# Kernel tuning notes

Hardware: AMD Instinct MI355X
Metric: run time of the kernel (lower is better)

The kernel has to match this reference:

```python
import jax, jax.numpy as jnp
import numpy as np

D_FEAT = 6
HID = 256
T = 60
B_DAYS = 4
STOCKS = 512
TRAIN_DAYS = 240
K_DAY = 10
N_NEIGHBOR = 10
SLOPE = 0.01  # nn.LeakyReLU default


def setup_inputs() -> dict:
    key = jax.random.key(0)
    ks = jax.random.split(key, 32)
    g = lambda i, shape, s=0.05: (jax.random.normal(ks[i], shape, dtype=jnp.float32) * s)
    inp = jax.random.normal(ks[0], (B_DAYS, STOCKS, D_FEAT * T), dtype=jnp.float32)
    train_hidden = jax.random.normal(ks[1], (TRAIN_DAYS, STOCKS, HID), dtype=jnp.float32)
    train_hidden_day = jax.random.normal(ks[2], (TRAIN_DAYS, HID), dtype=jnp.float32)
    return {
        "inp": inp,
        "train_hidden": train_hidden,
        "train_hidden_day": train_hidden_day,
        # GRU layer 0 (input D_FEAT) and layer 1 (input HID); gates [r,z,n] stacked -> 3*HID
        "W_ih0": g(3, (3 * HID, D_FEAT)), "W_hh0": g(4, (3 * HID, HID)),
        "b_ih0": g(5, (3 * HID,)), "b_hh0": g(6, (3 * HID,)),
        "W_ih1": g(7, (3 * HID, HID)), "W_hh1": g(8, (3 * HID, HID)),
        "b_ih1": g(9, (3 * HID,)), "b_hh1": g(10, (3 * HID,)),
        # lins MLP 256->512->512->256
        "lin0_W": g(11, (512, HID)), "lin0_b": g(12, (512,)),
        "lin1_W": g(13, (512, 512)), "lin1_b": g(14, (512,)),
        "lin2_W": g(15, (HID, 512)), "lin2_b": g(16, (HID,)),
        # projections (no bias) and output head
        "proj1_W": g(17, (HID, HID)), "proj2_W": g(18, (HID, HID)),
        "fc_W": g(19, (1, 2 * HID)), "fc_b": g(20, (1,)),
    }


def _leaky(x):
    return jnp.where(x >= 0, x, SLOPE * x)


def _gru_layer(x, W_ih, W_hh, b_ih, b_hh):
    # x: [N, T, in] -> [N, T, HID]
    xW = jnp.einsum('nti,gi->ntg', x, W_ih) + b_ih  # precompute input gates
    def step(h, xw):
        gh = h @ W_hh.T + b_hh
        xr, xz, xn = jnp.split(xw, 3, axis=-1)
        hr, hz, hn = jnp.split(gh, 3, axis=-1)
        r = jax.nn.sigmoid(xr + hr)
        z = jax.nn.sigmoid(xz + hz)
        n = jnp.tanh(xn + r * hn)
        h = (1.0 - z) * n + z * h
        return h, h
    h0 = jnp.zeros((x.shape[0], W_hh.shape[1]), x.dtype)
    _, hs = jax.lax.scan(step, h0, jnp.swapaxes(xW, 0, 1))
    return jnp.swapaxes(hs, 0, 1)


def _cos_sim(x, y):
    xy = x @ y.T
    xn = jnp.sqrt(jnp.sum(x * x, axis=1))[:, None]
    yn = jnp.sqrt(jnp.sum(y * y, axis=1))[:, None]
    cs = xy / (xn @ yn.T)
    return jnp.where(jnp.isnan(cs), 0.0, cs)


def reference(inp, train_hidden, train_hidden_day,
              W_ih0, W_hh0, b_ih0, b_hh0, W_ih1, W_hh1, b_ih1, b_hh1,
              lin0_W, lin0_b, lin1_W, lin1_b, lin2_W, lin2_b,
              proj1_W, proj2_W, fc_W, fc_b):
    B, S = inp.shape[0], inp.shape[1]
    x = inp.reshape(B * S, D_FEAT, -1).transpose(0, 2, 1)  # [N, T, d_feat]
    h = _gru_layer(x, W_ih0, W_hh0, b_ih0, b_hh0)
    h = _gru_layer(h, W_ih1, W_hh1, b_ih1, b_hh1)
    out = h[:, -1, :]                                      # [N, HID]
    mb = _leaky(out @ lin0_W.T + lin0_b)
    mb = _leaky(mb @ lin1_W.T + lin1_b)
    mb = _leaky(mb @ lin2_W.T + lin2_b)                    # mini_batch_out [N, HID]
    mb_day = jnp.mean(mb.reshape(B, S, -1), axis=1)        # [B, HID]
    day_sim = _cos_sim(mb_day, train_hidden_day)           # [B, TRAIN_DAYS]
    _, day_idx = jax.lax.top_k(day_sim, K_DAY)             # [B, K_DAY]
    sample = train_hidden[day_idx].reshape(-1, train_hidden.shape[-1])  # [B*K_DAY*S, HID]
    q = mb @ proj1_W.T
    kh = sample @ proj2_W.T
    cs = _cos_sim(q, kh)                                   # [N, B*K_DAY*S]
    vals, idx = jax.lax.top_k(cs, N_NEIGHBOR)              # per-row top-k (distinct cols)
    # sparse mask (ones/n_neighbor) * cos_sim, then sparse @ kh == weighted gather-sum
    agg = jnp.einsum('nk,nkh->nh', vals / N_NEIGHBOR, kh[idx])
    cat = jnp.concatenate([mb, agg], axis=1)               # [N, 2*HID]
    y = (cat @ fc_W.T + fc_b).squeeze(-1)
    return y.reshape(B, -1)
```

## Files before the change

### kernel.cpp

```cpp
#include <hip/hip_runtime.h>
#include <cmath>
#include <cstdint>

#define D_FEAT 6
#define T_SEQ  60
#define HID    256
#define G3     768
#define NROW   2048
#define NSAMP  20480

__device__ __forceinline__ float sigmoidf_(float x) { return 1.0f / (1.0f + expf(-x)); }

struct PrepArgs {
  const float* src[9];
  float* dst[9];
  int N[9], K[9], ro[9];
};

__global__ void prep_weights(PrepArgs a) {
  int seg = blockIdx.y;
  const float* S = a.src[seg];
  float* D = a.dst[seg];
  int N = a.N[seg], K = a.K[seg], ro = a.ro[seg];
  int total = N * K;
  for (int i = blockIdx.x * blockDim.x + threadIdx.x; i < total; i += gridDim.x * blockDim.x) {
    int n = i / K, k = i - n * K;
    D[(size_t)(k + ro) * N + n] = S[i];
  }
}

__device__ __forceinline__ void kloop256(const float* __restrict__ A,
                                         const float* __restrict__ B,
                                         float (&acc)[3][8])
{
  float4 Aa[4][2];
  float  Bb[2][12];
#pragma unroll
  for (int c = 0; c < 4; ++c) {
    Aa[c][0] = *(const float4*)(A + c * 8);
    Aa[c][1] = *(const float4*)(A + c * 8 + 4);
  }
#pragma unroll
  for (int c = 0; c < 4; ++c)
#pragma unroll
    for (int u = 0; u < 3; ++u)
      Bb[0][c * 3 + u] = B[(size_t)c * G3 + u * 256];

  for (int kb = 0; kb < 256; kb += 8) {
    {
      const float* p = B + (size_t)(kb + 4) * G3;
#pragma unroll
      for (int c = 0; c < 4; ++c)
#pragma unroll
        for (int u = 0; u < 3; ++u)
          Bb[1][c * 3 + u] = p[(size_t)c * G3 + u * 256];
    }
#pragma unroll
    for (int c = 0; c < 4; ++c) {
      float4 alo = Aa[c][0], ahi = Aa[c][1];
      int kn = kb + 4 + c;
      Aa[c][0] = *(const float4*)(A + kn * 8);
      Aa[c][1] = *(const float4*)(A + kn * 8 + 4);
#pragma unroll
      for (int u = 0; u < 3; ++u) {
        float b = Bb[0][c * 3 + u];
        acc[u][0] += alo.x * b; acc[u][1] += alo.y * b;
        acc[u][2] += alo.z * b; acc[u][3] += alo.w * b;
        acc[u][4] += ahi.x * b; acc[u][5] += ahi.y * b;
        acc[u][6] += ahi.z * b; acc[u][7] += ahi.w * b;
      }
    }
    {
      int kw = (kb + 8) & 255;
      const float* p = B + (size_t)kw * G3;
#pragma unroll
      for (int c = 0; c < 4; ++c)
#pragma unroll
        for (int u = 0; u < 3; ++u)
          Bb[0][c * 3 + u] = p[(size_t)c * G3 + u * 256];
    }
#pragma unroll
    for (int c = 0; c < 4; ++c) {
      float4 alo = Aa[c][0], ahi = Aa[c][1];
      int kn = (kb + 8 + c) & 255;
      Aa[c][0] = *(const float4*)(A + kn * 8);
      Aa[c][1] = *(const float4*)(A + kn * 8 + 4);
#pragma unroll
      for (int u = 0; u < 3; ++u) {
        float b = Bb[1][c * 3 + u];
        acc[u][0] += alo.x * b; acc[u][1] += alo.y * b;
        acc[u][2] += alo.z * b; acc[u][3] += alo.w * b;
        acc[u][4] += ahi.x * b; acc[u][5] += ahi.y * b;
        acc[u][6] += ahi.z * b; acc[u][7] += ahi.w * b;
      }
    }
  }
}

__global__ __launch_bounds__(256, 1)
void gru_fused(const float* __restrict__ inp, const float* __restrict__ WThh0,
               const float* __restrict__ WTcat, const float* __restrict__ WTih0,
               const float* __restrict__ bih0, const float* __restrict__ bhh0,
               const float* __restrict__ bih1, const float* __restrict__ bhh1,
               float* __restrict__ hrow)
{
  __shared__ float h0A[2048], h0B[2048];
  __shared__ float h1A[2048], h1B[2048];
  __shared__ float xls[2880];

  const int tid = threadIdx.x;
  const int m0 = blockIdx.x * 8;

  for (int c = tid; c < 2880; c += 256) {
    int row = c / 360, it = c - row * 360;
    xls[it * 8 + row] = inp[(size_t)(m0 + row) * 360 + it];
  }
  for (int c = tid; c < 2048; c += 256) { h0A[c] = 0.f; h1A[c] = 0.f; }

  float h0c[8], h1c[8];
#pragma unroll
  for (int r = 0; r < 8; ++r) { h0c[r] = 0.f; h1c[r] = 0.f; }

  float b_ih0[3], b_hh0[3], b_ih1[3], b_hh1[3];
#pragma unroll
  for (int u = 0; u < 3; ++u) {
    int o = u * 256 + tid;
    b_ih0[u] = bih0[o]; b_hh0[u] = bhh0[o];
    b_ih1[u] = bih1[o]; b_hh1[u] = bhh1[o];
  }
  __syncthreads();

  const float* Bhh0 = WThh0 + tid;
  const float* Bc0  = WTcat + tid;
  const float* Bc1  = WTcat + (size_t)256 * G3 + tid;

  for (int t = 0; t < T_SEQ; ++t) {
    const float* h0cur = (t & 1) ? h0B : h0A;
    float*       h0nxt = (t & 1) ? h0A : h0B;
    const float* h1cur = (t & 1) ? h1B : h1A;
    float*       h1nxt = (t & 1) ? h1A : h1B;

    float xw[3][8];
#pragma unroll
    for (int u = 0; u < 3; ++u)
#pragma unroll
      for (int r = 0; r < 8; ++r) xw[u][r] = b_ih0[u];
#pragma unroll
    for (int i = 0; i < 6; ++i) {
      float4 xlo = *(const float4*)&xls[(i * 60 + t) * 8];
      float4 xhi = *(const float4*)&xls[(i * 60 + t) * 8 + 4];
#pragma unroll
      for (int u = 0; u < 3; ++u) {
        float b = WTih0[i * G3 + u * 256 + tid];
        xw[u][0] += xlo.x * b; xw[u][1] += xlo.y * b;
        xw[u][2] += xlo.z * b; xw[u][3] += xlo.w * b;
        xw[u][4] += xhi.x * b; xw[u][5] += xhi.y * b;
        xw[u][6] += xhi.z * b; xw[u][7] += xhi.w * b;
      }
    }
    float gh[3][8];
#pragma unroll
    for (int u = 0; u < 3; ++u)
#pragma unroll
      for (int r = 0; r < 8; ++r) gh[u][r] = 0.f;
    kloop256(h0cur, Bhh0, gh);

    {
      float hn[8];
#pragma unroll
      for (int r = 0; r < 8; ++r) {
        float rr = sigmoidf_(xw[0][r] + (gh[0][r] + b_hh0[0]));
        float zz = sigmoidf_(xw[1][r] + (gh[1][r] + b_hh0[1]));
        float nn = tanhf(xw[2][r] + rr * (gh[2][r] + b_hh0[2]));
        h0c[r] = (1.f - zz) * nn + zz * h0c[r];
        hn[r] = h0c[r];
      }
      *(float4*)&h0nxt[tid * 8]     = *(float4*)&hn[0];
      *(float4*)&h0nxt[tid * 8 + 4] = *(float4*)&hn[4];
    }
    __syncthreads();

    float acc[3][8];
#pragma unroll
    for (int u = 0; u < 3; ++u)
#pragma unroll
      for (int r = 0; r < 8; ++r) acc[u][r] = 0.f;
    kloop256(h0nxt, Bc0, acc);
    float xn8[8];
#pragma unroll
    for (int r = 0; r < 8; ++r) { xn8[r] = acc[2][r]; acc[2][r] = 0.f; }
    kloop256(h1cur, Bc1, acc);

    {
      float hn[8];
#pragma unroll
      for (int r = 0; r < 8; ++r) {
        float rr = sigmoidf_((acc[0][r] + b_ih1[0]) + b_hh1[0]);
        float zz = sigmoidf_((acc[1][r] + b_ih1[1]) + b_hh1[1]);
        float nn = tanhf((xn8[r] + b_ih1[2]) + rr * (acc[2][r] + b_hh1[2]));
        h1c[r] = (1.f - zz) * nn + zz * h1c[r];
        hn[r] = h1c[r];
      }
      *(float4*)&h1nxt[tid * 8]     = *(float4*)&hn[0];
      *(float4*)&h1nxt[tid * 8 + 4] = *(float4*)&hn[4];
    }
    __syncthreads();
  }

#pragma unroll
  for (int r = 0; r < 8; ++r)
    hrow[(size_t)(m0 + r) * 256 + tid] = h1c[r];
}

__global__ __launch_bounds__(256, 2)
void gemm_act(const float* __restrict__ A, const int* __restrict__ rowsrc,
              const float* __restrict__ WT, const float* __restrict__ bias,
              float* __restrict__ C, int M, int N, int K, int act)
{
  __shared__ float4 As4[128 * 32];
  const int tx = threadIdx.x, ty = threadIdx.y;
  const int tid = ty * 32 + tx;
  const int n0 = blockIdx.x * 32, m0 = blockIdx.y * 32;
  const int K4 = K >> 2;

  for (int c = tid; c < K4 * 32; c += 256) {
    int k4 = c % K4, m = c / K4;
    int row = m0 + m;
    if (rowsrc) row = rowsrc[row];
    As4[k4 * 32 + m] = *(const float4*)(A + (size_t)row * K + k4 * 4);
  }
  __syncthreads();

  float acc[4] = {0,0,0,0};
  const int n = n0 + tx;
  const float* pb = WT + n;

  float bc[4], bn_[4];
#pragma unroll
  for (int kk = 0; kk < 4; ++kk) bc[kk] = pb[(size_t)kk * N];
  for (int k4 = 0; k4 < K4; ++k4) {
    int nk4 = (k4 + 1 < K4) ? (k4 + 1) : 0;
    const float* pn = pb + (size_t)nk4 * 4 * N;
#pragma unroll
    for (int kk = 0; kk < 4; ++kk) bn_[kk] = pn[(size_t)kk * N];
    float4 a0 = As4[k4 * 32 + ty * 4 + 0];
    float4 a1 = As4[k4 * 32 + ty * 4 + 1];
    float4 a2 = As4[k4 * 32 + ty * 4 + 2];
    float4 a3 = As4[k4 * 32 + ty * 4 + 3];
#pragma unroll
    for (int kk = 0; kk < 4; ++kk) {
      float b = bc[kk];
      acc[0] += ((const float*)&a0)[kk] * b;
      acc[1] += ((const float*)&a1)[kk] * b;
      acc[2] += ((const float*)&a2)[kk] * b;
      acc[3] += ((const float*)&a3)[kk] * b;
    }
#pragma unroll
    for (int q = 0; q < 4; ++q) bc[q] = bn_[q];
  }
  float bb = bias ? bias[n] : 0.f;
#pragma unroll
  for (int r = 0; r < 4; ++r) {
    float v = acc[r] + bb;
    if (act) v = (v >= 0.f) ? v : 0.01f * v;
    C[(size_t)(m0 + ty * 4 + r) * N + n] = v;
  }
}

__global__ void mbday_part(const float* __restrict__ mbf, float* __restrict__ part) {
  int d = blockIdx.x, sl = blockIdx.y, c = threadIdx.x;
  float s = 0.f;
  int base = d * 512 + sl * 64;
  for (int st = 0; st < 64; ++st) s += mbf[(size_t)(base + st) * 256 + c];
  part[(size_t)(d * 8 + sl) * 256 + c] = s;
}

__global__ void mbday_fin(const float* __restrict__ part, float* __restrict__ mbday) {
  int d = blockIdx.x, c = threadIdx.x;
  float s = 0.f;
#pragma unroll
  for (int p = 0; p < 8; ++p) s += part[(size_t)(d * 8 + p) * 256 + c];
  mbday[d * 256 + c] = s * (1.0f / 512.0f);
}

__global__ void daytopk_kernel(const float* __restrict__ mbday, const float* __restrict__ thd,
                               int* __restrict__ dayidx) {
  __shared__ float mbs[256];
  __shared__ float sim[256];
  __shared__ float red[256];
  __shared__ int   redi[256];
  const int d = blockIdx.x, t = threadIdx.x;
  mbs[t] = mbday[d * 256 + t];
  __syncthreads();
  red[t] = mbs[t] * mbs[t];
  __syncthreads();
  for (int o = 128; o; o >>= 1) { if (t < o) red[t] += red[t + o]; __syncthreads(); }
  float xn = sqrtf(red[0]);
  float v = -INFINITY;
  if (t < 240) {
    float dot = 0.f, yn2 = 0.f;
    for (int k = 0; k < 256; ++k) {
      float y = thd[t * 256 + k];
      dot += mbs[k] * y;
      yn2 += y * y;
    }
    float den = xn * sqrtf(yn2);
    v = (den > 0.f) ? dot / den : 0.f;
  }
  sim[t] = v;
  __syncthreads();
  for (int it = 0; it < 10; ++it) {
    red[t] = sim[t]; redi[t] = t;
    __syncthreads();
    for (int o = 128; o; o >>= 1) {
      if (t < o) {
        if (red[t + o] > red[t] || (red[t + o] == red[t] && redi[t + o] < redi[t])) {
          red[t] = red[t + o]; redi[t] = redi[t + o];
        }
      }
      __syncthreads();
    }
    if (t == 0) { int bi = redi[0]; dayidx[d * 10 + it] = bi; sim[bi] = -INFINITY; }
    __syncthreads();
  }
}

__global__ void rowsrc_kernel(const int* __restrict__ dayidx, int* __restrict__ rowsrc) {
  int r = blockIdx.x * 256 + threadIdx.x;
  if (r < NSAMP) rowsrc[r] = dayidx[r >> 9] * 512 + (r & 511);
}

__global__ void rownorm_kernel(const float* __restrict__ X, float* __restrict__ out, int rows) {
  int w = threadIdx.x >> 6;
  int lane = threadIdx.x & 63;
  int row = blockIdx.x * 4 + w;
  if (row >= rows) return;
  float4 x = *(const float4*)(X + (size_t)row * 256 + lane * 4);
  float s = x.x * x.x + x.y * x.y + x.z * x.z + x.w * x.w;
#pragma unroll
  for (int o = 32; o; o >>= 1) s += __shfl_down(s, o, 64);
  if (lane == 0) out[row] = sqrtf(s);
}

__global__ void qnorm_kernel(float* __restrict__ q, const float* __restrict__ qn) {
  int i = blockIdx.x * 256 + threadIdx.x;
  int row = i >> 8;
  float n = qn[row];
  q[i] = (n > 0.f) ? q[i] / n : 0.f;
}

__global__ void khT_kernel(const float* __restrict__ kh, const float* __restrict__ khn,
                           float* __restrict__ khT) {
  __shared__ float tile[32][33];
  int jb = blockIdx.x * 32;
  int kb = blockIdx.y * 32;
  int tx = threadIdx.x & 31, tyy = threadIdx.x >> 5;
  for (int rr = tyy; rr < 32; rr += 8) {
    float n = khn[jb + rr];
    float v = kh[(size_t)(jb + rr) * 256 + kb + tx];
    tile[rr][tx] = (n > 0.f) ? v / n : 0.f;
  }
  __syncthreads();
  for (int rr = tyy; rr < 32; rr += 8) {
    khT[(size_t)(kb + rr) * NSAMP + jb + tx] = tile[tx][rr];
  }
}

__global__ __launch_bounds__(256, 4)
void csmax_kernel(const float* __restrict__ qh, const float* __restrict__ khT,
                  float* __restrict__ topvp, int* __restrict__ topip)
{
  __shared__ float4 qs[256][2];
  __shared__ float csch[8 * 512];
  const int tid = threadIdx.x;
  const int split = blockIdx.x & 7;
  const int m0 = (blockIdx.x >> 3) * 8;
  {
    int k = tid;
    float4 v0, v1;
    v0.x = qh[(size_t)(m0 + 0) * 256 + k]; v0.y = qh[(size_t)(m0 + 1) * 256 + k];
    v0.z = qh[(size_t)(m0 + 2) * 256 + k]; v0.w = qh[(size_t)(m0 + 3) * 256 + k];
    v1.x = qh[(size_t)(m0 + 4) * 256 + k]; v1.y = qh[(size_t)(m0 + 5) * 256 + k];
    v1.z = qh[(size_t)(m0 + 6) * 256 + k]; v1.w = qh[(size_t)(m0 + 7) * 256 + k];
    qs[k][0] = v0; qs[k][1] = v1;
  }
  __syncthreads();
  const int lane = tid & 63;
  const int wv = tid >> 6;

  float tv0[10], tv1[10];
  int   tj0[10], tj1[10];
  int   tn0 = 0, tn1 = 0;
  float tmv0 = -INFINITY, tmv1 = -INFINITY;
  int   tmi0 = 0, tmi1 = 0;

  auto process_row = [&](int r, float (&tv)[10], int (&tj)[10], int& tn,
                         float& tmv, int& tmi, int jb) {
    float4 c0 = *(const float4*)&csch[r * 512 + lane * 8];
    float4 c1 = *(const float4*)&csch[r * 512 + lane * 8 + 4];
    float cv[8] = {c0.x, c0.y, c0.z, c0.w, c1.x, c1.y, c1.z, c1.w};
    const int cj0 = jb + lane * 8;
    while (true) {
      float bv = -INFINITY; int bj = 0x7fffffff;
#pragma unroll
      for (int u = 0; u < 8; ++u) {
        if (cv[u] > bv) { bv = cv[u]; bj = cj0 + u; }
      }
#pragma unroll
      for (int o = 32; o; o >>= 1) {
        float ov = __shfl_down(bv, o, 64);
        int   oj = __shfl_down(bj, o, 64);
        if (ov > bv || (ov == bv && oj < bj)) { bv = ov; bj = oj; }
      }
      bv = __shfl(bv, 0, 64); bj = __shfl(bj, 0, 64);
      bool take;
      if (tn < 10) take = true;
      else take = (bv > tmv) || (bv == tmv && bj < tmi);
      if (!take) break;
      if (tn < 10) {
#pragma unroll
        for (int s = 0; s < 10; ++s) if (s == tn) { tv[s] = bv; tj[s] = bj; }
        tn++;
        if (tn == 10) {
          float mv = tv[0]; int mi = tj[0];
#pragma unroll
          for (int s = 1; s < 10; ++s) {
            bool w = (tv[s] < mv) || (tv[s] == mv && tj[s] > mi);
            if (w) { mv = tv[s]; mi = tj[s]; }
          }
          tmv = mv; tmi = mi;
        }
      } else {
        int ms = 0; float mv = tv[0]; int mi = tj[0];
#pragma unroll
        for (int s = 1; s < 10; ++s) {
          bool w = (tv[s] < mv) || (tv[s] == mv && tj[s] > mi);
          if (w) { ms = s; mv = tv[s]; mi = tj[s]; }
        }
#pragma unroll
        for (int s = 0; s < 10; ++s) if (s == ms) { tv[s] = bv; tj[s] = bj; }
        mv = tv[0]; mi = tj[0];
#pragma unroll
        for (int s = 1; s < 10; ++s) {
          bool w = (tv[s] < mv) || (tv[s] == mv && tj[s] > mi);
          if (w) { mv = tv[s]; mi = tj[s]; }
        }
        tmv = mv; tmi = mi;
      }
#pragma unroll
      for (int u = 0; u < 8; ++u) if (cj0 + u == bj) cv[u] = -INFINITY;
    }
  };

  for (int ci = 0; ci < 5; ++ci) {
    const int ch = split * 5 + ci;
    const int jb = ch * 512;
    float acc[8][2];
#pragma unroll
    for (int r = 0; r < 8; ++r) { acc[r][0] = 0.f; acc[r][1] = 0.f; }
    const float* kp = khT + jb + tid;

    float b0c[4], b1c[4], b0n[4], b1n[4];
#pragma unroll
    for (int kk = 0; kk < 4; ++kk) {
      b0c[kk] = kp[(size_t)kk * NSAMP];
      b1c[kk] = kp[(size_t)kk * NSAMP + 256];
    }
    for (int k4 = 0; k4 < 64; ++k4) {
      int nk4 = (k4 + 1) & 63;
      const float* pn = kp + (size_t)nk4 * 4 * NSAMP;
#pragma unroll
      for (int kk = 0; kk < 4; ++kk) {
        b0n[kk] = pn[(size_t)kk * NSAMP];
        b1n[kk] = pn[(size_t)kk * NSAMP + 256];
      }
#pragma unroll
      for (int kk = 0; kk < 4; ++kk) {
        float4 qa = qs[k4 * 4 + kk][0];
        float4 qb = qs[k4 * 4 + kk][1];
        float b0 = b0c[kk], b1 = b1c[kk];
        acc[0][0] += qa.x * b0; acc[1][0] += qa.y * b0; acc[2][0] += qa.z * b0; acc[3][0] += qa.w * b0;
        acc[4][0] += qb.x * b0; acc[5][0] += qb.y * b0; acc[6][0] += qb.z * b0; acc[7][0] += qb.w * b0;
        acc[0][1] += qa.x * b1; acc[1][1] += qa.y * b1; acc[2][1] += qa.z * b1; acc[3][1] += qa.w * b1;
        acc[4][1] += qb.x * b1; acc[5][1] += qb.y * b1; acc[6][1] += qb.z * b1; acc[7][1] += qb.w * b1;
      }
#pragma unroll
      for (int q = 0; q < 4; ++q) { b0c[q] = b0n[q]; b1c[q] = b1n[q]; }
    }
    __syncthreads();
#pragma unroll
    for (int r = 0; r < 8; ++r) {
      csch[r * 512 + tid] = acc[r][0];
      csch[r * 512 + 256 + tid] = acc[r][1];
    }
    __syncthreads();
    process_row(wv,     tv0, tj0, tn0, tmv0, tmi0, jb);
    process_row(wv + 4, tv1, tj1, tn1, tmv1, tmi1, jb);
  }
  __syncthreads();

  if (lane == 0) {
    int row0 = m0 + wv;
#pragma unroll
    for (int s = 0; s < 10; ++s) {
      topvp[(size_t)row0 * 80 + split * 10 + s] = tv0[s];
      topip[(size_t)row0 * 80 + split * 10 + s] = tj0[s];
    }
    int row1 = m0 + wv + 4;
#pragma unroll
    for (int s = 0; s < 10; ++s) {
      topvp[(size_t)row1 * 80 + split * 10 + s] = tv1[s];
      topip[(size_t)row1 * 80 + split * 10 + s] = tj1[s];
    }
  }
}

__global__ void merge_topk(const float* __restrict__ topvp, const int* __restrict__ topip,
                           float* __restrict__ topv, int* __restrict__ topi)
{
  const int wv = threadIdx.x >> 6;
  const int lane = threadIdx.x & 63;
  const int row = blockIdx.x * 4 + wv;
  float v0 = topvp[(size_t)row * 80 + lane];
  int   i0 = topip[(size_t)row * 80 + lane];
  float v1 = (lane < 16) ? topvp[(size_t)row * 80 + 64 + lane] : -INFINITY;
  int   i1 = (lane < 16) ? topip[(size_t)row * 80 + 64 + lane] : 0x7fffffff;
  for (int s = 0; s < 10; ++s) {
    float bv = v0; int bj = i0;
    if (v1 > bv || (v1 == bv && i1 < bj)) { bv = v1; bj = i1; }
#pragma unroll
    for (int o = 1; o < 64; o <<= 1) {
      float ov = __shfl_xor(bv, o, 64);
      int   oj = __shfl_xor(bj, o, 64);
      if (ov > bv || (ov == bv && oj < bj)) { bv = ov; bj = oj; }
    }
    if (lane == 0) { topv[row * 10 + s] = bv; topi[row * 10 + s] = bj; }
    if (i0 == bj) { v0 = -INFINITY; i0 = 0x7fffffff; }
    if (i1 == bj) { v1 = -INFINITY; i1 = 0x7fffffff; }
  }
}

__global__ void final_kernel(const float* __restrict__ mb, const float* __restrict__ kh,
                             const float* __restrict__ topv, const int* __restrict__ topi,
                             const float* __restrict__ fcW, const float* __restrict__ fcb,
                             float* __restrict__ y)
{
  __shared__ float red[256];
  int n = blockIdx.x, c = threadIdx.x;
  float agg = 0.f;
#pragma unroll
  for (int k = 0; k < 10; ++k) {
    float w = topv[n * 10 + k] / 10.0f;
    int idx = topi[n * 10 + k];
    agg += w * kh[(size_t)idx * 256 + c];
  }
  float val = fcW[c] * mb[(size_t)n * 256 + c] + fcW[256 + c] * agg;
  red[c] = val;
  __syncthreads();
  for (int o = 128; o; o >>= 1) { if (c < o) red[c] += red[c + o]; __syncthreads(); }
  if (c == 0) y[n] = red[0] + fcb[0];
}

extern "C" void kernel_launch(void* const* d_in, const int* in_sizes, int n_in,
                              void* d_out, int out_size, void* d_ws, size_t ws_size,
                              hipStream_t stream)
{
  const float* inp    = (const float*)d_in[0];
  const float* trainh = (const float*)d_in[1];
  const float* thd    = (const float*)d_in[2];
  const float* Wih0   = (const float*)d_in[3];
  const float* Whh0   = (const float*)d_in[4];
  const float* bih0   = (const float*)d_in[5];
  const float* bhh0   = (const float*)d_in[6];
  const float* Wih1   = (const float*)d_in[7];
  const float* Whh1   = (const float*)d_in[8];
  const float* bih1   = (const float*)d_in[9];
  const float* bhh1   = (const float*)d_in[10];
  const float* lin0W  = (const float*)d_in[11];
  const float* lin0b  = (const float*)d_in[12];
  const float* lin1W  = (const float*)d_in[13];
  const float* lin1b  = (const float*)d_in[14];
  const float* lin2W  = (const float*)d_in[15];
  const float* lin2b  = (const float*)d_in[16];
  const float* p1W    = (const float*)d_in[17];
  const float* p2W    = (const float*)d_in[18];
  const float* fcW    = (const float*)d_in[19];
  const float* fcb    = (const float*)d_in[20];

  float* ws = (float*)d_ws;
  float* WT_hh0 = ws + 0;
  float* WTcat  = ws + 196608;
  float* WT_l0  = ws + 589824;
  float* WT_l1  = ws + 720896;
  float* WT_l2  = ws + 983040;
  float* WT_p1  = ws + 1114112;
  float* WT_p2  = ws + 1179648;
  float* hrow   = ws + 1245184;
  float* mb1    = ws + 3342336;
  float* mb2    = ws + 4390912;
  float* mbf    = ws + 5439488;
  float* mbday  = ws + 5963776;
  float* qbuf   = ws + 5964800;
  float* kh     = ws + 6489088;
  float* khT    = ws + 11731968;
  float* khn    = ws + 16974848;
  float* qn     = ws + 16995328;
  float* topv   = ws + 16997376;
  int*   dayidx = (int*)(ws + 17017856);
  int*   rowsrc = (int*)(ws + 17017920);
  int*   topi   = (int*)(ws + 17038400);
  float* topvp  = mb1;
  int*   topip  = (int*)(mb1 + 163840);
  float* WT_ih0 = mb2;
  float* mbpart = mb2;

  PrepArgs pa;
  pa.src[0] = Whh0;  pa.dst[0] = WT_hh0; pa.N[0] = 768; pa.K[0] = 256; pa.ro[0] = 0;
  pa.src[1] = Wih1;  pa.dst[1] = WTcat;  pa.N[1] = 768; pa.K[1] = 256; pa.ro[1] = 0;
  pa.src[2] = Whh1;  pa.dst[2] = WTcat;  pa.N[2] = 768; pa.K[2] = 256; pa.ro[2] = 256;
  pa.src[3] = lin0W; pa.dst[3] = WT_l0;  pa.N[3] = 512; pa.K[3] = 256; pa.ro[3] = 0;
  pa.src[4] = lin1W; pa.dst[4] = WT_l1;  pa.N[4] = 512; pa.K[4] = 512; pa.ro[4] = 0;
  pa.src[5] = lin2W; pa.dst[5] = WT_l2;  pa.N[5] = 256; pa.K[5] = 512; pa.ro[5] = 0;
  pa.src[6] = p1W;   pa.dst[6] = WT_p1;  pa.N[6] = 256; pa.K[6] = 256; pa.ro[6] = 0;
  pa.src[7] = p2W;   pa.dst[7] = WT_p2;  pa.N[7] = 256; pa.K[7] = 256; pa.ro[7] = 0;
  pa.src[8] = Wih0;  pa.dst[8] = WT_ih0; pa.N[8] = 768; pa.K[8] = 6;   pa.ro[8] = 0;
  prep_weights<<<dim3(64, 9), dim3(256), 0, stream>>>(pa);

  gru_fused<<<256, 256, 0, stream>>>(inp, WT_hh0, WTcat, WT_ih0, bih0, bhh0, bih1, bhh1, hrow);

  gemm_act<<<dim3(16, 64), dim3(32, 8), 0, stream>>>(hrow, nullptr, WT_l0, lin0b, mb1, 2048, 512, 256, 1);
  gemm_act<<<dim3(16, 64), dim3(32, 8), 0, stream>>>(mb1, nullptr, WT_l1, lin1b, mb2, 2048, 512, 512, 1);
  gemm_act<<<dim3(8, 64),  dim3(32, 8), 0, stream>>>(mb2, nullptr, WT_l2, lin2b, mbf, 2048, 256, 512, 1);

  mbday_part<<<dim3(4, 8), 256, 0, stream>>>(mbf, mbpart);
  mbday_fin<<<4, 256, 0, stream>>>(mbpart, mbday);
  daytopk_kernel<<<4, 256, 0, stream>>>(mbday, thd, dayidx);
  rowsrc_kernel<<<80, 256, 0, stream>>>(dayidx, rowsrc);

  gemm_act<<<dim3(8, 640), dim3(32, 8), 0, stream>>>(trainh, rowsrc, WT_p2, nullptr, kh, 20480, 256, 256, 0);
  gemm_act<<<dim3(8, 64),  dim3(32, 8), 0, stream>>>(mbf, nullptr, WT_p1, nullptr, qbuf, 2048, 256, 256, 0);

  rownorm_kernel<<<5120, 256, 0, stream>>>(kh, khn, 20480);
  rownorm_kernel<<<512, 256, 0, stream>>>(qbuf, qn, 2048);
  qnorm_kernel<<<2048, 256, 0, stream>>>(qbuf, qn);
  khT_kernel<<<dim3(640, 8), 256, 0, stream>>>(kh, khn, khT);

  csmax_kernel<<<2048, 256, 0, stream>>>(qbuf, khT, topvp, topip);
  merge_topk<<<512, 256, 0, stream>>>(topvp, topip, topv, topi);
  final_kernel<<<2048, 256, 0, stream>>>(mbf, kh, topv, topi, fcW, fcb, (float*)d_out);

  (void)in_sizes; (void)n_in; (void)out_size; (void)ws_size;
}
```

Before: 3.799 ms.

## Split GRU recurrent K-reduction across two thread halves with shared-memory exchange

The fused GRU kernel now launches 512 threads per block. Each half computes a 128-wide slice of the hidden-dimension reduction, and the partial sums are combined through a padded shared-memory exchange buffer. This doubles the wavefronts per CU so the latency-bound recurrent matvec gets more parallelism. In exchange it adds two extra block-wide barriers per timestep and leaves the upper half idle during the gate nonlinearities.

```diff
diff --git a/kernel.cpp b/kernel.cpp
--- a/kernel.cpp
+++ b/kernel.cpp
@@ -29,7 +29,7 @@
   }
 }
 
-__device__ __forceinline__ void kloop256(const float* __restrict__ A,
+__device__ __forceinline__ void kloop128(const float* __restrict__ A,
                                          const float* __restrict__ B,
                                          float (&acc)[3][8])
 {
@@ -46,7 +46,7 @@
     for (int u = 0; u < 3; ++u)
       Bb[0][c * 3 + u] = B[(size_t)c * G3 + u * 256];
 
-  for (int kb = 0; kb < 256; kb += 8) {
+  for (int kb = 0; kb < 128; kb += 8) {
     {
       const float* p = B + (size_t)(kb + 4) * G3;
 #pragma unroll
@@ -71,7 +71,7 @@
       }
     }
     {
-      int kw = (kb + 8) & 255;
+      int kw = (kb + 8) & 127;
       const float* p = B + (size_t)kw * G3;
 #pragma unroll
       for (int c = 0; c < 4; ++c)
@@ -82,7 +82,7 @@
 #pragma unroll
     for (int c = 0; c < 4; ++c) {
       float4 alo = Aa[c][0], ahi = Aa[c][1];
-      int kn = (kb + 8 + c) & 255;
+      int kn = (kb + 8 + c) & 127;
       Aa[c][0] = *(const float4*)(A + kn * 8);
       Aa[c][1] = *(const float4*)(A + kn * 8 + 4);
 #pragma unroll
@@ -97,7 +97,7 @@
   }
 }
 
-__global__ __launch_bounds__(256, 1)
+__global__ __launch_bounds__(512, 1)
 void gru_fused(const float* __restrict__ inp, const float* __restrict__ WThh0,
                const float* __restrict__ WTcat, const float* __restrict__ WTih0,
                const float* __restrict__ bih0, const float* __restrict__ bhh0,
@@ -107,15 +107,18 @@
   __shared__ float h0A[2048], h0B[2048];
   __shared__ float h1A[2048], h1B[2048];
   __shared__ float xls[2880];
+  __shared__ float exch[256 * 33];
 
   const int tid = threadIdx.x;
+  const int col = tid & 255;
+  const int half = tid >> 8;
   const int m0 = blockIdx.x * 8;
 
-  for (int c = tid; c < 2880; c += 256) {
+  for (int c = tid; c < 2880; c += 512) {
     int row = c / 360, it = c - row * 360;
     xls[it * 8 + row] = inp[(size_t)(m0 + row) * 360 + it];
   }
-  for (int c = tid; c < 2048; c += 256) { h0A[c] = 0.f; h1A[c] = 0.f; }
+  for (int c = tid; c < 2048; c += 512) { h0A[c] = 0.f; h1A[c] = 0.f; }
 
   float h0c[8], h1c[8];
 #pragma unroll
@@ -124,15 +127,17 @@
   float b_ih0[3], b_hh0[3], b_ih1[3], b_hh1[3];
 #pragma unroll
   for (int u = 0; u < 3; ++u) {
-    int o = u * 256 + tid;
+    int o = u * 256 + col;
     b_ih0[u] = bih0[o]; b_hh0[u] = bhh0[o];
     b_ih1[u] = bih1[o]; b_hh1[u] = bhh1[o];
   }
   __syncthreads();
 
-  const float* Bhh0 = WThh0 + tid;
-  const float* Bc0  = WTcat + tid;
-  const float* Bc1  = WTcat + (size_t)256 * G3 + tid;
+  const int aoff = half * 1024;
+  const float* Bhh0 = WThh0 + (size_t)(half * 128) * G3 + col;
+  const float* Bc0  = WTcat + (size_t)(half * 128) * G3 + col;
+  const float* Bc1  = WTcat + (size_t)(256 + half * 128) * G3 + col;
+  float* exc = exch + col * 33;
 
   for (int t = 0; t < T_SEQ; ++t) {
     const float* h0cur = (t & 1) ? h0B : h0A;
@@ -140,43 +145,55 @@
     const float* h1cur = (t & 1) ? h1B : h1A;
     float*       h1nxt = (t & 1) ? h1A : h1B;
 
+    float gh[3][8];
+#pragma unroll
+    for (int u = 0; u < 3; ++u)
+#pragma unroll
+      for (int r = 0; r < 8; ++r) gh[u][r] = 0.f;
+    kloop128(h0cur + aoff, Bhh0, gh);
+
     float xw[3][8];
-#pragma unroll
-    for (int u = 0; u < 3; ++u)
-#pragma unroll
-      for (int r = 0; r < 8; ++r) xw[u][r] = b_ih0[u];
-#pragma unroll
-    for (int i = 0; i < 6; ++i) {
-      float4 xlo = *(const float4*)&xls[(i * 60 + t) * 8];
-      float4 xhi = *(const float4*)&xls[(i * 60 + t) * 8 + 4];
-#pragma unroll
-      for (int u = 0; u < 3; ++u) {
-        float b = WTih0[i * G3 + u * 256 + tid];
-        xw[u][0] += xlo.x * b; xw[u][1] += xlo.y * b;
-        xw[u][2] += xlo.z * b; xw[u][3] += xlo.w * b;
-        xw[u][4] += xhi.x * b; xw[u][5] += xhi.y * b;
-        xw[u][6] += xhi.z * b; xw[u][7] += xhi.w * b;
-      }
-    }
-    float gh[3][8];
-#pragma unroll
-    for (int u = 0; u < 3; ++u)
-#pragma unroll
-      for (int r = 0; r < 8; ++r) gh[u][r] = 0.f;
-    kloop256(h0cur, Bhh0, gh);
-
-    {
+    if (half == 0) {
+#pragma unroll
+      for (int u = 0; u < 3; ++u)
+#pragma unroll
+        for (int r = 0; r < 8; ++r) xw[u][r] = b_ih0[u];
+#pragma unroll
+      for (int i = 0; i < 6; ++i) {
+        float4 xlo = *(const float4*)&xls[(i * 60 + t) * 8];
+        float4 xhi = *(const float4*)&xls[(i * 60 + t) * 8 + 4];
+#pragma unroll
+        for (int u = 0; u < 3; ++u) {
+          float b = WTih0[i * G3 + u * 256 + col];
+          xw[u][0] += xlo.x * b; xw[u][1] += xlo.y * b;
+          xw[u][2] += xlo.z * b; xw[u][3] += xlo.w * b;
+          xw[u][4] += xhi.x * b; xw[u][5] += xhi.y * b;
+          xw[u][6] += xhi.z * b; xw[u][7] += xhi.w * b;
+        }
+      }
+    } else {
+#pragma unroll
+      for (int u = 0; u < 3; ++u)
+#pragma unroll
+        for (int r = 0; r < 8; ++r) exc[u * 8 + r] = gh[u][r];
+    }
+    __syncthreads();
+
+    if (half == 0) {
       float hn[8];
 #pragma unroll
       for (int r = 0; r < 8; ++r) {
-        float rr = sigmoidf_(xw[0][r] + (gh[0][r] + b_hh0[0]));
-        float zz = sigmoidf_(xw[1][r] + (gh[1][r] + b_hh0[1]));
-        float nn = tanhf(xw[2][r] + rr * (gh[2][r] + b_hh0[2]));
+        float g0 = gh[0][r] + exc[r];
+        float g1 = gh[1][r] + exc[8 + r];
+        float g2 = gh[2][r] + exc[16 + r];
+        float rr = sigmoidf_(xw[0][r] + (g0 + b_hh0[0]));
+        float zz = sigmoidf_(xw[1][r] + (g1 + b_hh0[1]));
+        float nn = tanhf(xw[2][r] + rr * (g2 + b_hh0[2]));
         h0c[r] = (1.f - zz) * nn + zz * h0c[r];
         hn[r] = h0c[r];
       }
-      *(float4*)&h0nxt[tid * 8]     = *(float4*)&hn[0];
-      *(float4*)&h0nxt[tid * 8 + 4] = *(float4*)&hn[4];
+      *(float4*)&h0nxt[col * 8]     = *(float4*)&hn[0];
+      *(float4*)&h0nxt[col * 8 + 4] = *(float4*)&hn[4];
     }
     __syncthreads();
 
@@ -185,31 +202,48 @@
     for (int u = 0; u < 3; ++u)
 #pragma unroll
       for (int r = 0; r < 8; ++r) acc[u][r] = 0.f;
-    kloop256(h0nxt, Bc0, acc);
+    kloop128(h0nxt + aoff, Bc0, acc);
     float xn8[8];
 #pragma unroll
     for (int r = 0; r < 8; ++r) { xn8[r] = acc[2][r]; acc[2][r] = 0.f; }
-    kloop256(h1cur, Bc1, acc);
-
-    {
+    kloop128(h1cur + aoff, Bc1, acc);
+
+    if (half == 1) {
+#pragma unroll
+      for (int r = 0; r < 8; ++r) {
+        exc[r]      = acc[0][r];
+        exc[8 + r]  = acc[1][r];
+        exc[16 + r] = xn8[r];
+        exc[24 + r] = acc[2][r];
+      }
+    }
+    __syncthreads();
+
+    if (half == 0) {
       float hn[8];
 #pragma unroll
       for (int r = 0; r < 8; ++r) {
-        float rr = sigmoidf_((acc[0][r] + b_ih1[0]) + b_hh1[0]);
-        float zz = sigmoidf_((acc[1][r] + b_ih1[1]) + b_hh1[1]);
-        float nn = tanhf((xn8[r] + b_ih1[2]) + rr * (acc[2][r] + b_hh1[2]));
+        float ra = acc[0][r] + exc[r];
+        float za = acc[1][r] + exc[8 + r];
+        float xa = xn8[r] + exc[16 + r];
+        float ha = acc[2][r] + exc[24 + r];
+        float rr = sigmoidf_((ra + b_ih1[0]) + b_hh1[0]);
+        float zz = sigmoidf_((za + b_ih1[1]) + b_hh1[1]);
+        float nn = tanhf((xa + b_ih1[2]) + rr * (ha + b_hh1[2]));
         h1c[r] = (1.f - zz) * nn + zz * h1c[r];
         hn[r] = h1c[r];
       }
-      *(float4*)&h1nxt[tid * 8]     = *(float4*)&hn[0];
-      *(float4*)&h1nxt[tid * 8 + 4] = *(float4*)&hn[4];
-    }
-    __syncthreads();
-  }
-
-#pragma unroll
-  for (int r = 0; r < 8; ++r)
-    hrow[(size_t)(m0 + r) * 256 + tid] = h1c[r];
+      *(float4*)&h1nxt[col * 8]     = *(float4*)&hn[0];
+      *(float4*)&h1nxt[col * 8 + 4] = *(float4*)&hn[4];
+    }
+    __syncthreads();
+  }
+
+  if (half == 0) {
+#pragma unroll
+    for (int r = 0; r < 8; ++r)
+      hrow[(size_t)(m0 + r) * 256 + col] = h1c[r];
+  }
 }
 
 __global__ __launch_bounds__(256, 2)
@@ -626,7 +660,7 @@
   pa.src[8] = Wih0;  pa.dst[8] = WT_ih0; pa.N[8] = 768; pa.K[8] = 6;   pa.ro[8] = 0;
   prep_weights<<<dim3(64, 9), dim3(256), 0, stream>>>(pa);
 
-  gru_fused<<<256, 256, 0, stream>>>(inp, WT_hh0, WTcat, WT_ih0, bih0, bhh0, bih1, bhh1, hrow);
+  gru_fused<<<256, 512, 0, stream>>>(inp, WT_hh0, WTcat, WT_ih0, bih0, bhh0, bih1, bhh1, hrow);
 
   gemm_act<<<dim3(16, 64), dim3(32, 8), 0, stream>>>(hrow, nullptr, WT_l0, lin0b, mb1, 2048, 512, 256, 1);
   gemm_act<<<dim3(16, 64), dim3(32, 8), 0, stream>>>(mb1, nullptr, WT_l1, lin1b, mb2, 2048, 512, 512, 1);
```

Result: faster. 3.283 ms (-13.6%).
